# Optimization experiments

Hardware: AMD Instinct MI355X
Metric: run time of the kernel (lower is better)

Reference implementation:

```python
import jax, jax.numpy as jnp
import numpy as np

EPS = 1e-6


def softmax_kernel_transformation(data, is_query, projection_matrix):
    # data: [B,L,H,D], projection_matrix: [M,D]
    d = data.shape[-1]
    m = projection_matrix.shape[0]
    data_normalizer = 1.0 / jnp.sqrt(jnp.sqrt(jnp.float32(d)))
    data = data_normalizer * data
    ratio = 1.0 / jnp.sqrt(jnp.float32(m))
    data_dash = jnp.einsum('blhd,md->blhm', data, projection_matrix)
    diag_data = jnp.sum(jnp.square(data), axis=-1, keepdims=True) / 2.0  # [B,L,H,1]
    if is_query:
        stab = jnp.max(data_dash, axis=-1, keepdims=True)  # per-position max over M
    else:
        stab = jnp.max(data_dash, axis=(1, 3), keepdims=True)  # max over L and M
    return ratio * (jnp.exp(data_dash - diag_data - stab) + EPS)


def causal_linear_attention(qp, kp, v):
    # qp,kp: [L,B,H,M]; v: [L,B,H,D]. Sequential prefix-sum recurrence (FAVOR+ causal).
    B, H, M = qp.shape[1], qp.shape[2], qp.shape[3]
    D = v.shape[-1]
    kv0 = jnp.zeros((B, H, M, D), dtype=v.dtype)
    ks0 = jnp.zeros((B, H, M), dtype=kp.dtype)

    def step(carry, inp):
        kv_sum, k_sum = carry
        q_t, k_t, v_t = inp  # [B,H,M], [B,H,M], [B,H,D]
        kv_sum = kv_sum + jnp.einsum('bhm,bhd->bhmd', k_t, v_t)
        k_sum = k_sum + k_t
        num_t = jnp.einsum('bhmd,bhm->bhd', kv_sum, q_t)  # numerator row
        den_t = jnp.einsum('bhm,bhm->bh', q_t, k_sum)     # normalizer row
        return (kv_sum, k_sum), (num_t, den_t)

    (_, _), (num, den) = jax.lax.scan(step, (kv0, ks0), (qp, kp, v))
    return num, den  # [L,B,H,D], [L,B,H]


def favor_attention(query, key, value, projection_matrix):
    query_prime = softmax_kernel_transformation(query, True, projection_matrix)   # [B,L,H,M]
    key_prime = softmax_kernel_transformation(key, False, projection_matrix)      # [B,L,H,M]
    qp = jnp.transpose(query_prime, (1, 0, 2, 3))  # [L,B,H,M]
    kp = jnp.transpose(key_prime, (1, 0, 2, 3))
    v = jnp.transpose(value, (1, 0, 2, 3))         # [L,B,H,D]
    num, den = causal_linear_attention(qp, kp, v)
    av = jnp.transpose(num, (1, 0, 2, 3))          # [B,L,H,D]
    norm = jnp.transpose(den, (1, 0, 2))[..., None]  # [B,L,H,1]
    return av / norm


def setup_inputs() -> dict:
    B, L, H, D, M = 2, 2048, 8, 64, 128
    root = jax.random.key(0)
    kq, kk, kv, kp = jax.random.split(root, 4)
    return {
        'query': jax.random.normal(kq, (B, L, H, D), dtype=jnp.float32),
        'key': jax.random.normal(kk, (B, L, H, D), dtype=jnp.float32),
        'value': jax.random.normal(kv, (B, L, H, D), dtype=jnp.float32),
        'projection_matrix': jax.random.normal(kp, (M, D), dtype=jnp.float32),
    }


def reference(query, key, value, projection_matrix):
    return favor_attention(query, key, value, projection_matrix)
```

## Files before the change

kernel.cpp:

```cpp
#include <hip/hip_runtime.h>
#include <math.h>

typedef __attribute__((ext_vector_type(8))) short short8;
typedef __attribute__((ext_vector_type(4))) float f32x4;
typedef __attribute__((ext_vector_type(4))) unsigned short u16x4;

constexpr int B_ = 2, L_ = 2048, H_ = 8, D_ = 64, M_ = 128;
constexpr int T_ = 64;
constexpr int C_ = L_ / T_;
constexpr float DN_ = 0.35355339059327373f;
constexpr float RATIO_ = 0.08838834764831845f;
constexpr float EPSV_ = 1e-6f;
constexpr float REPS_ = RATIO_ * EPSV_;
constexpr float KEPS_ = 64.0f * REPS_;


__device__ inline unsigned short f2bf(float x) {
  const unsigned u = __float_as_uint(x);
  return (unsigned short)((u + 0x7fffu + ((u >> 16) & 1u)) >> 16);
}
__device__ inline float bf2f(unsigned short h) {
  return __uint_as_float(((unsigned)h) << 16);
}

__global__ __launch_bounds__(256) void feat_kernel(
    const float* __restrict__ q, const float* __restrict__ k,
    const float* __restrict__ P, const float* __restrict__ v,
    unsigned short* __restrict__ qp16, unsigned short* __restrict__ kp16,
    unsigned short* __restrict__ kvc16, float* __restrict__ ksc,
    unsigned short* __restrict__ vt16, float* __restrict__ blockmax,
    float* __restrict__ vsum) {
  __shared__ __align__(16) unsigned short xh_s[T_][72];
  __shared__ __align__(16) unsigned short xl_s[T_][72];
  __shared__ __align__(16) unsigned short ph_s[M_][72];
  __shared__ __align__(16) unsigned short pl_s[M_][72];
  __shared__ float diag_s[T_];
  __shared__ float wred_s[2][T_];
  __shared__ float red4_s[4];
  unsigned short (*kpT_s)[72] = ph_s;
  unsigned short (*vt_s)[72] = xh_s;

  const int bid = blockIdx.x;
  const bool isQ = bid < 512;
  const int sub = isQ ? bid : bid - 512;
  const int c = sub % C_, bh = sub / C_;
  const int b = bh >> 3, h = bh & 7;
  const float* x = isQ ? q : k;
  const int tid = threadIdx.x;
  const int w = tid >> 6, lane = tid & 63;
  const int l15 = lane & 15, l16 = lane >> 4;

  if (tid < T_) diag_s[tid] = 0.f;
  __syncthreads();
  for (int i4 = tid; i4 < T_ * 16; i4 += 256) {
    const int r = i4 >> 4, d0 = (i4 & 15) * 4;
    f32x4 t4 = *reinterpret_cast<const f32x4*>(
        &x[((size_t)(b * L_ + c * T_ + r) * H_ + h) * D_ + d0]);
    u16x4 hi, lo;
    float sq = 0.f;
#pragma unroll
    for (int j = 0; j < 4; ++j) {
      const float xv = t4[j] * DN_;
      sq += xv * xv;
      const unsigned short hb = f2bf(xv);
      hi[j] = hb;
      lo[j] = f2bf(xv - bf2f(hb));
    }
    *reinterpret_cast<u16x4*>(&xh_s[r][d0]) = hi;
    *reinterpret_cast<u16x4*>(&xl_s[r][d0]) = lo;
    atomicAdd(&diag_s[r], sq);
  }
  for (int i4 = tid; i4 < M_ * 16; i4 += 256) {
    const int m = i4 >> 4, d0 = (i4 & 15) * 4;
    const f32x4 t4 = *reinterpret_cast<const f32x4*>(&P[m * D_ + d0]);
    u16x4 hi, lo;
#pragma unroll
    for (int j = 0; j < 4; ++j) {
      const unsigned short hb = f2bf(t4[j]);
      hi[j] = hb;
      lo[j] = f2bf(t4[j] - bf2f(hb));
    }
    *reinterpret_cast<u16x4*>(&ph_s[m][d0]) = hi;
    *reinterpret_cast<u16x4*>(&pl_s[m][d0]) = lo;
  }
  __syncthreads();

  const int rblk = (w >> 1) * 32, cblk = (w & 1) * 64;
  f32x4 acc[2][4];
#pragma unroll
  for (int i = 0; i < 2; ++i)
#pragma unroll
    for (int j = 0; j < 4; ++j) acc[i][j] = {0.f, 0.f, 0.f, 0.f};
#pragma unroll
  for (int kk = 0; kk < 2; ++kk) {
    short8 ah[2], al[2], bh8[4], bl8[4];
#pragma unroll
    for (int ti = 0; ti < 2; ++ti) {
      ah[ti] = *reinterpret_cast<const short8*>(
          &xh_s[rblk + ti * 16 + l15][kk * 32 + l16 * 8]);
      al[ti] = *reinterpret_cast<const short8*>(
          &xl_s[rblk + ti * 16 + l15][kk * 32 + l16 * 8]);
    }
#pragma unroll
    for (int tj = 0; tj < 4; ++tj) {
      bh8[tj] = *reinterpret_cast<const short8*>(
          &ph_s[cblk + tj * 16 + l15][kk * 32 + l16 * 8]);
      bl8[tj] = *reinterpret_cast<const short8*>(
          &pl_s[cblk + tj * 16 + l15][kk * 32 + l16 * 8]);
    }
#pragma unroll
    for (int ti = 0; ti < 2; ++ti)
#pragma unroll
      for (int tj = 0; tj < 4; ++tj) {
        acc[ti][tj] = __builtin_amdgcn_mfma_f32_16x16x32_bf16(
            al[ti], bh8[tj], acc[ti][tj], 0, 0, 0);
        acc[ti][tj] = __builtin_amdgcn_mfma_f32_16x16x32_bf16(
            ah[ti], bl8[tj], acc[ti][tj], 0, 0, 0);
        acc[ti][tj] = __builtin_amdgcn_mfma_f32_16x16x32_bf16(
            ah[ti], bh8[tj], acc[ti][tj], 0, 0, 0);
      }
  }

  if (isQ) {
    float rmax[2][4];
#pragma unroll
    for (int ti = 0; ti < 2; ++ti)
#pragma unroll
      for (int j = 0; j < 4; ++j) {
        float m0 = fmaxf(fmaxf(acc[ti][0][j], acc[ti][1][j]),
                         fmaxf(acc[ti][2][j], acc[ti][3][j]));
#pragma unroll
        for (int off = 1; off < 16; off <<= 1)
          m0 = fmaxf(m0, __shfl_xor(m0, off, 64));
        rmax[ti][j] = m0;
      }
    if (l15 == 0) {
#pragma unroll
      for (int ti = 0; ti < 2; ++ti)
#pragma unroll
        for (int j = 0; j < 4; ++j)
          wred_s[w & 1][rblk + ti * 16 + l16 * 4 + j] = rmax[ti][j];
    }
    __syncthreads();
    unsigned short* outr = qp16 + ((size_t)bh * L_ + c * T_) * M_;
#pragma unroll
    for (int ti = 0; ti < 2; ++ti)
#pragma unroll
      for (int j = 0; j < 4; ++j) {
        const int row = rblk + ti * 16 + l16 * 4 + j;
        const float sub2 =
            0.5f * diag_s[row] + fmaxf(wred_s[0][row], wred_s[1][row]);
#pragma unroll
        for (int tj = 0; tj < 4; ++tj) {
          const int col = cblk + tj * 16 + l15;
          outr[row * M_ + col] =
              f2bf(RATIO_ * (expf(acc[ti][tj][j] - sub2) + EPSV_));
        }
      }
  } else {
    float bm = -INFINITY;
#pragma unroll
    for (int ti = 0; ti < 2; ++ti)
#pragma unroll
      for (int tj = 0; tj < 4; ++tj)
#pragma unroll
        for (int j = 0; j < 4; ++j) bm = fmaxf(bm, acc[ti][tj][j]);
#pragma unroll
    for (int off = 1; off < 64; off <<= 1)
      bm = fmaxf(bm, __shfl_xor(bm, off, 64));
    if (lane == 0) red4_s[w] = bm;
    __syncthreads();
    const float lmax =
        fmaxf(fmaxf(red4_s[0], red4_s[1]), fmaxf(red4_s[2], red4_s[3]));
    if (tid == 0) blockmax[sub] = lmax;

    unsigned short* kpr = kp16 + ((size_t)bh * L_ + c * T_) * M_;
#pragma unroll
    for (int ti = 0; ti < 2; ++ti)
#pragma unroll
      for (int j = 0; j < 4; ++j) {
        const int row = rblk + ti * 16 + l16 * 4 + j;
        const float sub2 = 0.5f * diag_s[row] + lmax;
#pragma unroll
        for (int tj = 0; tj < 4; ++tj) {
          const int col = cblk + tj * 16 + l15;
          const unsigned short us = f2bf(RATIO_ * expf(acc[ti][tj][j] - sub2));
          kpr[row * M_ + col] = us;
          kpT_s[col][row] = us;
        }
      }
    for (int i = tid; i < T_ * D_; i += 256) {
      const int t = i & 63, d = i >> 6;
      vt_s[d][t] = f2bf(v[((size_t)(b * L_ + c * T_ + t) * H_ + h) * D_ + d]);
    }
    __syncthreads();

    unsigned short* vg = vt16 + (size_t)(bh * C_ + c) * (D_ * T_);
    for (int i8 = tid; i8 < D_ * 8; i8 += 256) {
      const int d = i8 >> 3, t0 = (i8 & 7) * 8;
      *reinterpret_cast<short8*>(&vg[d * T_ + t0]) =
          *reinterpret_cast<const short8*>(&vt_s[d][t0]);
    }
    if (tid < M_) {
      float s = 0.f;
      for (int t = 0; t < T_; ++t) s += bf2f(kpT_s[tid][t]);
      ksc[(size_t)(bh * C_ + c) * M_ + tid] = s;
    }
    if (tid >= 128 && tid < 128 + D_) {
      const int d = tid - 128;
      float s = 0.f;
      for (int t = 0; t < T_; ++t) s += bf2f(vt_s[d][t]);
      vsum[(size_t)(bh * C_ + c) * D_ + d] = s;
    }
    f32x4 acc2[2][4];
#pragma unroll
    for (int i = 0; i < 2; ++i)
#pragma unroll
      for (int j = 0; j < 4; ++j) acc2[i][j] = {0.f, 0.f, 0.f, 0.f};
#pragma unroll
    for (int kk = 0; kk < 2; ++kk) {
      short8 av[2], bv[4];
#pragma unroll
      for (int ti = 0; ti < 2; ++ti)
        av[ti] = *reinterpret_cast<const short8*>(
            &vt_s[rblk + ti * 16 + l15][kk * 32 + l16 * 8]);
#pragma unroll
      for (int tj = 0; tj < 4; ++tj)
        bv[tj] = *reinterpret_cast<const short8*>(
            &kpT_s[cblk + tj * 16 + l15][kk * 32 + l16 * 8]);
#pragma unroll
      for (int ti = 0; ti < 2; ++ti)
#pragma unroll
        for (int tj = 0; tj < 4; ++tj)
          acc2[ti][tj] = __builtin_amdgcn_mfma_f32_16x16x32_bf16(
              av[ti], bv[tj], acc2[ti][tj], 0, 0, 0);
    }
    unsigned short* ob = kvc16 + (size_t)(bh * C_ + c) * (M_ * D_);
#pragma unroll
    for (int ti = 0; ti < 2; ++ti)
#pragma unroll
      for (int j = 0; j < 4; ++j) {
        const int row = rblk + ti * 16 + l16 * 4 + j;
#pragma unroll
        for (int tj = 0; tj < 4; ++tj) {
          const int col = cblk + tj * 16 + l15;
          ob[row * M_ + col] = f2bf(acc2[ti][tj][j]);
        }
      }
  }
}

__global__ __launch_bounds__(256) void prefix_kernel(
    const unsigned short* __restrict__ kvc16,
    unsigned short* __restrict__ kvp16, float* __restrict__ ksc,
    const float* __restrict__ blockmax, const float* __restrict__ vsum) {
  __shared__ float bm_s[C_];
  __shared__ float sc_s[C_];
  __shared__ float vs_s[2][C_];
  const int bid = blockIdx.x;
  const int ej = bid & 31, bh = bid >> 5;
  if (threadIdx.x < C_) bm_s[threadIdx.x] = blockmax[bh * C_ + threadIdx.x];
  if (threadIdx.x >= 64 && threadIdx.x < 64 + 2 * C_) {
    const int t = threadIdx.x - 64;
    const int ld = t >> 5, cc = t & 31;
    vs_s[ld][cc] = vsum[(size_t)(bh * C_ + cc) * D_ + ej * 2 + ld];
  }
  __syncthreads();
  if (threadIdx.x < C_) {
    float km = -INFINITY;
#pragma unroll
    for (int cc = 0; cc < C_; ++cc) km = fmaxf(km, bm_s[cc]);
    sc_s[threadIdx.x] = expf(bm_s[threadIdx.x] - km);
  }
  __syncthreads();
  const int e = ej * 256 + threadIdx.x;
  const int dl = threadIdx.x >> 7;
  float vals[C_];
#pragma unroll
  for (int cc = 0; cc < C_; ++cc)
    vals[cc] = bf2f(kvc16[(size_t)(bh * C_ + cc) * (M_ * D_) + e]) * sc_s[cc] +
               REPS_ * vs_s[dl][cc];
  float run = 0.f;
#pragma unroll
  for (int cc = 0; cc < C_; ++cc) {
    const float t = vals[cc];
    vals[cc] = run;
    run += t;
  }
#pragma unroll
  for (int cc = 0; cc < C_; ++cc)
    kvp16[(size_t)(bh * C_ + cc) * (M_ * D_) + e] = f2bf(vals[cc]);
  if (ej == 0 && threadIdx.x < M_) {
    const int m = threadIdx.x;
    float ks[C_];
#pragma unroll
    for (int cc = 0; cc < C_; ++cc)
      ks[cc] = ksc[(size_t)(bh * C_ + cc) * M_ + m] * sc_s[cc] + KEPS_;
    float rs = 0.f;
#pragma unroll
    for (int cc = 0; cc < C_; ++cc) {
      const float t = ks[cc];
      ks[cc] = rs;
      rs += t;
    }
#pragma unroll
    for (int cc = 0; cc < C_; ++cc)
      ksc[(size_t)(bh * C_ + cc) * M_ + m] = ks[cc];
  }
}

__global__ __launch_bounds__(256) void intra_kernel(
    const unsigned short* __restrict__ qp16,
    const unsigned short* __restrict__ kp16,
    const unsigned short* __restrict__ vt16,
    const unsigned short* __restrict__ kvp16, const float* __restrict__ ksp,
    const float* __restrict__ blockmax, float* __restrict__ out) {
  __shared__ __align__(16) unsigned short qp_s[T_][136];
  __shared__ __align__(16) unsigned short kp_s[T_][136];
  __shared__ __align__(16) unsigned short kvp_s[D_][136];
  __shared__ __align__(16) unsigned short S_s[T_][72];
  __shared__ __align__(16) unsigned short vt_s[D_][72];
  __shared__ float ksp_s[M_];
  __shared__ float denp_s[4][T_];
  __shared__ float qsump_s[4][T_];
  __shared__ float den_s[T_];
  __shared__ float bm_s[C_];

  const int bid = blockIdx.x;
  const int c = bid % C_, bh = bid / C_;
  const int b = bh >> 3, h = bh & 7;
  const int tid = threadIdx.x;
  const int w = tid >> 6, lane = tid & 63;
  const int l15 = lane & 15, l16 = lane >> 4;

  const unsigned short* qpt = qp16 + ((size_t)bh * L_ + c * T_) * M_;
  const unsigned short* kpt = kp16 + ((size_t)bh * L_ + c * T_) * M_;
  const unsigned short* kvt = kvp16 + (size_t)(bh * C_ + c) * (M_ * D_);
  const unsigned short* vg = vt16 + (size_t)(bh * C_ + c) * (D_ * T_);

  if (tid < C_) bm_s[tid] = blockmax[bh * C_ + tid];
  for (int i8 = tid; i8 < T_ * 16; i8 += 256) {
    const int r = i8 >> 4, m0 = (i8 & 15) * 8;
    *reinterpret_cast<short8*>(&qp_s[r][m0]) =
        *reinterpret_cast<const short8*>(&qpt[r * M_ + m0]);
    *reinterpret_cast<short8*>(&kp_s[r][m0]) =
        *reinterpret_cast<const short8*>(&kpt[r * M_ + m0]);
    *reinterpret_cast<short8*>(&kvp_s[r][m0]) =
        *reinterpret_cast<const short8*>(&kvt[r * M_ + m0]);
  }
  for (int i8 = tid; i8 < D_ * 8; i8 += 256) {
    const int d = i8 >> 3, t0 = (i8 & 7) * 8;
    *reinterpret_cast<short8*>(&vt_s[d][t0]) =
        *reinterpret_cast<const short8*>(&vg[d * T_ + t0]);
  }
  if (tid < M_) ksp_s[tid] = ksp[(size_t)(bh * C_ + c) * M_ + tid];
  __syncthreads();

  {
    const int t = lane;
    float p = 0.f;
    for (int m = w * 32; m < w * 32 + 32; ++m) p += bf2f(qp_s[t][m]);
    qsump_s[w][t] = p;
  }
  __syncthreads();

  float km = -INFINITY;
#pragma unroll
  for (int cc = 0; cc < C_; ++cc) km = fmaxf(km, bm_s[cc]);
  const float sc = expf(bm_s[c] - km);

  const int rblk = (w >> 1) * 32, cblk = (w & 1) * 32;
  f32x4 Sacc[2][2];
#pragma unroll
  for (int i = 0; i < 2; ++i)
#pragma unroll
    for (int j = 0; j < 2; ++j) Sacc[i][j] = {0.f, 0.f, 0.f, 0.f};

#pragma unroll
  for (int kk = 0; kk < 4; ++kk) {
    short8 af[2], bf[2];
#pragma unroll
    for (int ti = 0; ti < 2; ++ti)
      af[ti] = *reinterpret_cast<const short8*>(
          &qp_s[rblk + ti * 16 + l15][kk * 32 + l16 * 8]);
#pragma unroll
    for (int tj = 0; tj < 2; ++tj)
      bf[tj] = *reinterpret_cast<const short8*>(
          &kp_s[cblk + tj * 16 + l15][kk * 32 + l16 * 8]);
#pragma unroll
    for (int ti = 0; ti < 2; ++ti)
#pragma unroll
      for (int tj = 0; tj < 2; ++tj)
        Sacc[ti][tj] = __builtin_amdgcn_mfma_f32_16x16x32_bf16(
            af[ti], bf[tj], Sacc[ti][tj], 0, 0, 0);
  }
#pragma unroll
  for (int ti = 0; ti < 2; ++ti)
#pragma unroll
    for (int tj = 0; tj < 2; ++tj)
#pragma unroll
      for (int j = 0; j < 4; ++j) {
        const int row = rblk + ti * 16 + l16 * 4 + j;
        const int col = cblk + tj * 16 + l15;
        const float add = REPS_ * (qsump_s[0][row] + qsump_s[1][row] +
                                   qsump_s[2][row] + qsump_s[3][row]);
        const float sv = (col <= row) ? Sacc[ti][tj][j] * sc + add : 0.f;
        S_s[row][col] = f2bf(sv);
      }
  __syncthreads();

  {
    const int t = lane;
    float p = 0.f;
    if (w == 0) {
      for (int tp = 0; tp < 32; ++tp) p += bf2f(S_s[t][tp]);
    } else if (w == 1) {
      for (int tp = 32; tp < 64; ++tp) p += bf2f(S_s[t][tp]);
    } else if (w == 2) {
      for (int m = 0; m < 64; ++m) p += bf2f(qp_s[t][m]) * ksp_s[m];
    } else {
      for (int m = 64; m < 128; ++m) p += bf2f(qp_s[t][m]) * ksp_s[m];
    }
    denp_s[w][t] = p;
  }
  __syncthreads();
  if (tid < T_)
    den_s[tid] =
        denp_s[0][tid] + denp_s[1][tid] + denp_s[2][tid] + denp_s[3][tid];
  __syncthreads();

  const int dblk = (w & 1) * 32;
  f32x4 Nacc[2][2];
#pragma unroll
  for (int i = 0; i < 2; ++i)
#pragma unroll
    for (int j = 0; j < 2; ++j) Nacc[i][j] = {0.f, 0.f, 0.f, 0.f};

#pragma unroll
  for (int kk = 0; kk < 2; ++kk) {
    short8 af[2], bf[2];
#pragma unroll
    for (int ti = 0; ti < 2; ++ti)
      af[ti] = *reinterpret_cast<const short8*>(
          &S_s[rblk + ti * 16 + l15][kk * 32 + l16 * 8]);
#pragma unroll
    for (int tj = 0; tj < 2; ++tj)
      bf[tj] = *reinterpret_cast<const short8*>(
          &vt_s[dblk + tj * 16 + l15][kk * 32 + l16 * 8]);
#pragma unroll
    for (int ti = 0; ti < 2; ++ti)
#pragma unroll
      for (int tj = 0; tj < 2; ++tj)
        Nacc[ti][tj] = __builtin_amdgcn_mfma_f32_16x16x32_bf16(
            af[ti], bf[tj], Nacc[ti][tj], 0, 0, 0);
  }
#pragma unroll
  for (int kk = 0; kk < 4; ++kk) {
    short8 af[2], bf[2];
#pragma unroll
    for (int ti = 0; ti < 2; ++ti)
      af[ti] = *reinterpret_cast<const short8*>(
          &qp_s[rblk + ti * 16 + l15][kk * 32 + l16 * 8]);
#pragma unroll
    for (int tj = 0; tj < 2; ++tj)
      bf[tj] = *reinterpret_cast<const short8*>(
          &kvp_s[dblk + tj * 16 + l15][kk * 32 + l16 * 8]);
#pragma unroll
    for (int ti = 0; ti < 2; ++ti)
#pragma unroll
      for (int tj = 0; tj < 2; ++tj)
        Nacc[ti][tj] = __builtin_amdgcn_mfma_f32_16x16x32_bf16(
            af[ti], bf[tj], Nacc[ti][tj], 0, 0, 0);
  }

#pragma unroll
  for (int ti = 0; ti < 2; ++ti)
#pragma unroll
    for (int j = 0; j < 4; ++j) {
      const int row = rblk + ti * 16 + l16 * 4 + j;
      const float r = 1.f / den_s[row];
      float* orow = out + ((size_t)(b * L_ + c * T_ + row) * H_ + h) * D_;
#pragma unroll
      for (int tj = 0; tj < 2; ++tj) {
        const int col = dblk + tj * 16 + l15;
        orow[col] = Nacc[ti][tj][j] * r;
      }
    }
}

extern "C" void kernel_launch(void* const* d_in, const int* in_sizes, int n_in,
                              void* d_out, int out_size, void* d_ws,
                              size_t ws_size, hipStream_t stream) {
  const float* q = (const float*)d_in[0];
  const float* k = (const float*)d_in[1];
  const float* v = (const float*)d_in[2];
  const float* P = (const float*)d_in[3];
  float* out = (float*)d_out;

  float* ws = (float*)d_ws;
  float* blockmax = ws;
  float* ksp = blockmax + 512;
  float* vsum = ksp + (size_t)B_ * H_ * C_ * M_;
  unsigned short* qp16 = (unsigned short*)(vsum + (size_t)B_ * H_ * C_ * D_);
  unsigned short* kp16 = qp16 + (size_t)B_ * H_ * L_ * M_;
  unsigned short* kvc16 = kp16 + (size_t)B_ * H_ * L_ * M_;
  unsigned short* kvp16 = kvc16 + (size_t)B_ * H_ * C_ * D_ * M_;
  unsigned short* vt16 = kvp16 + (size_t)B_ * H_ * C_ * D_ * M_;

  feat_kernel<<<2 * B_ * H_ * C_, 256, 0, stream>>>(
      q, k, P, v, qp16, kp16, kvc16, ksp, vt16, blockmax, vsum);
  prefix_kernel<<<B_ * H_ * 32, 256, 0, stream>>>(kvc16, kvp16, ksp, blockmax,
                                                  vsum);
  intra_kernel<<<B_ * H_ * C_, 256, 0, stream>>>(qp16, kp16, vt16, kvp16, ksp,
                                                 blockmax, out);
}
```

Measured before the change: 48.22 us.

## Merge Q and K feature blocks, pre-split projection, stage outputs through LDS

Adds a small kernel that splits the projection matrix into bf16 hi/lo once, so the per-block split work goes away. feat_kernel now handles both the query and key tiles of a chunk in one block, with half the grid and a shared LDS buffer. It also replaces atomic diag accumulation with shuffle reductions and writes qp/kvc through LDS as vectorized stores. intra_kernel drops the LDS staging of kvp and v, reads them straight from global, and sets a launch bound for 3 blocks per SM. The merge halves parallelism and lengthens each feat block, and the global reads in the MFMA loop may be slower than LDS reads.

Measured after the change: 48.64 us. No clear change (+0.9%).

```diff
diff --git a/kernel.cpp b/kernel.cpp
--- a/kernel.cpp
+++ b/kernel.cpp
@@ -14,7 +14,6 @@
 constexpr float REPS_ = RATIO_ * EPSV_;
 constexpr float KEPS_ = 64.0f * REPS_;
 
-
 __device__ inline unsigned short f2bf(float x) {
   const unsigned u = __float_as_uint(x);
   return (unsigned short)((u + 0x7fffu + ((u >> 16) & 1u)) >> 16);
@@ -23,105 +22,106 @@
   return __uint_as_float(((unsigned)h) << 16);
 }
 
+__global__ __launch_bounds__(256) void psplit_kernel(
+    const float* __restrict__ P, unsigned short* __restrict__ Ph,
+    unsigned short* __restrict__ Pl) {
+  const int i = blockIdx.x * 256 + threadIdx.x;
+  const f32x4 t4 = *reinterpret_cast<const f32x4*>(&P[(size_t)i * 4]);
+  u16x4 hi, lo;
+#pragma unroll
+  for (int j = 0; j < 4; ++j) {
+    hi[j] = f2bf(t4[j]);
+    lo[j] = f2bf(t4[j] - bf2f(hi[j]));
+  }
+  *reinterpret_cast<u16x4*>(&Ph[(size_t)i * 4]) = hi;
+  *reinterpret_cast<u16x4*>(&Pl[(size_t)i * 4]) = lo;
+}
+
 __global__ __launch_bounds__(256) void feat_kernel(
     const float* __restrict__ q, const float* __restrict__ k,
-    const float* __restrict__ P, const float* __restrict__ v,
-    unsigned short* __restrict__ qp16, unsigned short* __restrict__ kp16,
-    unsigned short* __restrict__ kvc16, float* __restrict__ ksc,
-    unsigned short* __restrict__ vt16, float* __restrict__ blockmax,
-    float* __restrict__ vsum) {
-  __shared__ __align__(16) unsigned short xh_s[T_][72];
-  __shared__ __align__(16) unsigned short xl_s[T_][72];
-  __shared__ __align__(16) unsigned short ph_s[M_][72];
-  __shared__ __align__(16) unsigned short pl_s[M_][72];
+    const unsigned short* __restrict__ Ph, const unsigned short* __restrict__ Pl,
+    const float* __restrict__ v, unsigned short* __restrict__ qp16,
+    unsigned short* __restrict__ kp16, unsigned short* __restrict__ kvc16,
+    float* __restrict__ ksc, unsigned short* __restrict__ vt16,
+    float* __restrict__ blockmax, float* __restrict__ vsum) {
+  __shared__ __align__(16) unsigned short sm[27648];
   __shared__ float diag_s[T_];
   __shared__ float wred_s[2][T_];
   __shared__ float red4_s[4];
-  unsigned short (*kpT_s)[72] = ph_s;
-  unsigned short (*vt_s)[72] = xh_s;
-
-  const int bid = blockIdx.x;
-  const bool isQ = bid < 512;
-  const int sub = isQ ? bid : bid - 512;
+
+  const int sub = blockIdx.x;
   const int c = sub % C_, bh = sub / C_;
   const int b = bh >> 3, h = bh & 7;
-  const float* x = isQ ? q : k;
   const int tid = threadIdx.x;
   const int w = tid >> 6, lane = tid & 63;
   const int l15 = lane & 15, l16 = lane >> 4;
-
-  if (tid < T_) diag_s[tid] = 0.f;
-  __syncthreads();
-  for (int i4 = tid; i4 < T_ * 16; i4 += 256) {
-    const int r = i4 >> 4, d0 = (i4 & 15) * 4;
-    f32x4 t4 = *reinterpret_cast<const f32x4*>(
-        &x[((size_t)(b * L_ + c * T_ + r) * H_ + h) * D_ + d0]);
-    u16x4 hi, lo;
-    float sq = 0.f;
-#pragma unroll
-    for (int j = 0; j < 4; ++j) {
-      const float xv = t4[j] * DN_;
-      sq += xv * xv;
-      const unsigned short hb = f2bf(xv);
-      hi[j] = hb;
-      lo[j] = f2bf(xv - bf2f(hb));
-    }
-    *reinterpret_cast<u16x4*>(&xh_s[r][d0]) = hi;
-    *reinterpret_cast<u16x4*>(&xl_s[r][d0]) = lo;
-    atomicAdd(&diag_s[r], sq);
-  }
-  for (int i4 = tid; i4 < M_ * 16; i4 += 256) {
-    const int m = i4 >> 4, d0 = (i4 & 15) * 4;
-    const f32x4 t4 = *reinterpret_cast<const f32x4*>(&P[m * D_ + d0]);
-    u16x4 hi, lo;
-#pragma unroll
-    for (int j = 0; j < 4; ++j) {
-      const unsigned short hb = f2bf(t4[j]);
-      hi[j] = hb;
-      lo[j] = f2bf(t4[j] - bf2f(hb));
-    }
-    *reinterpret_cast<u16x4*>(&ph_s[m][d0]) = hi;
-    *reinterpret_cast<u16x4*>(&pl_s[m][d0]) = lo;
-  }
-  __syncthreads();
-
   const int rblk = (w >> 1) * 32, cblk = (w & 1) * 64;
+
+  for (int i8 = tid; i8 < M_ * 8; i8 += 256) {
+    const int m = i8 >> 3, d0 = (i8 & 7) * 8;
+    *reinterpret_cast<short8*>(&sm[9216 + m * 72 + d0]) =
+        *reinterpret_cast<const short8*>(&Ph[m * D_ + d0]);
+    *reinterpret_cast<short8*>(&sm[18432 + m * 72 + d0]) =
+        *reinterpret_cast<const short8*>(&Pl[m * D_ + d0]);
+  }
+
+#define STAGE_X(xptr)                                                         \
+  for (int i4 = tid; i4 < T_ * 16; i4 += 256) {                               \
+    const int r = i4 >> 4, d0 = (i4 & 15) * 4;                                \
+    f32x4 t4 = *reinterpret_cast<const f32x4*>(                               \
+        &(xptr)[((size_t)(b * L_ + c * T_ + r) * H_ + h) * D_ + d0]);         \
+    u16x4 hi, lo;                                                             \
+    float sq = 0.f;                                                           \
+    _Pragma("unroll") for (int j = 0; j < 4; ++j) {                           \
+      const float xv = t4[j] * DN_;                                           \
+      sq += xv * xv;                                                          \
+      const unsigned short hb = f2bf(xv);                                     \
+      hi[j] = hb;                                                             \
+      lo[j] = f2bf(xv - bf2f(hb));                                            \
+    }                                                                         \
+    *reinterpret_cast<u16x4*>(&sm[r * 72 + d0]) = hi;                         \
+    *reinterpret_cast<u16x4*>(&sm[4608 + r * 72 + d0]) = lo;                  \
+    _Pragma("unroll") for (int off = 1; off < 16; off <<= 1)                  \
+        sq += __shfl_xor(sq, off, 64);                                        \
+    if ((tid & 15) == 0) diag_s[r] = sq;                                      \
+  }
+
+#define DASH_MFMA(accv)                                                       \
+  _Pragma("unroll") for (int kk = 0; kk < 2; ++kk) {                          \
+    short8 ah[2], al[2], bh8[4], bl8[4];                                      \
+    _Pragma("unroll") for (int ti = 0; ti < 2; ++ti) {                        \
+      ah[ti] = *reinterpret_cast<const short8*>(                              \
+          &sm[(rblk + ti * 16 + l15) * 72 + kk * 32 + l16 * 8]);              \
+      al[ti] = *reinterpret_cast<const short8*>(                              \
+          &sm[4608 + (rblk + ti * 16 + l15) * 72 + kk * 32 + l16 * 8]);       \
+    }                                                                         \
+    _Pragma("unroll") for (int tj = 0; tj < 4; ++tj) {                        \
+      bh8[tj] = *reinterpret_cast<const short8*>(                             \
+          &sm[9216 + (cblk + tj * 16 + l15) * 72 + kk * 32 + l16 * 8]);       \
+      bl8[tj] = *reinterpret_cast<const short8*>(                             \
+          &sm[18432 + (cblk + tj * 16 + l15) * 72 + kk * 32 + l16 * 8]);      \
+    }                                                                         \
+    _Pragma("unroll") for (int ti = 0; ti < 2; ++ti)                          \
+        _Pragma("unroll") for (int tj = 0; tj < 4; ++tj) {                    \
+      accv[ti][tj] = __builtin_amdgcn_mfma_f32_16x16x32_bf16(                 \
+          al[ti], bh8[tj], accv[ti][tj], 0, 0, 0);                            \
+      accv[ti][tj] = __builtin_amdgcn_mfma_f32_16x16x32_bf16(                 \
+          ah[ti], bl8[tj], accv[ti][tj], 0, 0, 0);                            \
+      accv[ti][tj] = __builtin_amdgcn_mfma_f32_16x16x32_bf16(                 \
+          ah[ti], bh8[tj], accv[ti][tj], 0, 0, 0);                            \
+    }                                                                         \
+  }
+
+  STAGE_X(q);
+  __syncthreads();
   f32x4 acc[2][4];
 #pragma unroll
   for (int i = 0; i < 2; ++i)
 #pragma unroll
     for (int j = 0; j < 4; ++j) acc[i][j] = {0.f, 0.f, 0.f, 0.f};
-#pragma unroll
-  for (int kk = 0; kk < 2; ++kk) {
-    short8 ah[2], al[2], bh8[4], bl8[4];
-#pragma unroll
-    for (int ti = 0; ti < 2; ++ti) {
-      ah[ti] = *reinterpret_cast<const short8*>(
-          &xh_s[rblk + ti * 16 + l15][kk * 32 + l16 * 8]);
-      al[ti] = *reinterpret_cast<const short8*>(
-          &xl_s[rblk + ti * 16 + l15][kk * 32 + l16 * 8]);
-    }
-#pragma unroll
-    for (int tj = 0; tj < 4; ++tj) {
-      bh8[tj] = *reinterpret_cast<const short8*>(
-          &ph_s[cblk + tj * 16 + l15][kk * 32 + l16 * 8]);
-      bl8[tj] = *reinterpret_cast<const short8*>(
-          &pl_s[cblk + tj * 16 + l15][kk * 32 + l16 * 8]);
-    }
-#pragma unroll
-    for (int ti = 0; ti < 2; ++ti)
-#pragma unroll
-      for (int tj = 0; tj < 4; ++tj) {
-        acc[ti][tj] = __builtin_amdgcn_mfma_f32_16x16x32_bf16(
-            al[ti], bh8[tj], acc[ti][tj], 0, 0, 0);
-        acc[ti][tj] = __builtin_amdgcn_mfma_f32_16x16x32_bf16(
-            ah[ti], bl8[tj], acc[ti][tj], 0, 0, 0);
-        acc[ti][tj] = __builtin_amdgcn_mfma_f32_16x16x32_bf16(
-            ah[ti], bh8[tj], acc[ti][tj], 0, 0, 0);
-      }
-  }
-
-  if (isQ) {
+  DASH_MFMA(acc);
+
+  {
     float rmax[2][4];
 #pragma unroll
     for (int ti = 0; ti < 2; ++ti)
@@ -142,7 +142,6 @@
           wred_s[w & 1][rblk + ti * 16 + l16 * 4 + j] = rmax[ti][j];
     }
     __syncthreads();
-    unsigned short* outr = qp16 + ((size_t)bh * L_ + c * T_) * M_;
 #pragma unroll
     for (int ti = 0; ti < 2; ++ti)
 #pragma unroll
@@ -153,101 +152,136 @@
 #pragma unroll
         for (int tj = 0; tj < 4; ++tj) {
           const int col = cblk + tj * 16 + l15;
-          outr[row * M_ + col] =
+          sm[row * 136 + col] =
               f2bf(RATIO_ * (expf(acc[ti][tj][j] - sub2) + EPSV_));
         }
       }
-  } else {
-    float bm = -INFINITY;
+    __syncthreads();
+    unsigned short* outr = qp16 + ((size_t)bh * L_ + c * T_) * M_;
+    for (int i8 = tid; i8 < T_ * 16; i8 += 256) {
+      const int row = i8 >> 4, m0 = (i8 & 15) * 8;
+      *reinterpret_cast<short8*>(&outr[row * M_ + m0]) =
+          *reinterpret_cast<const short8*>(&sm[row * 136 + m0]);
+    }
+  }
+  __syncthreads();
+
+  STAGE_X(k);
+  __syncthreads();
+#pragma unroll
+  for (int i = 0; i < 2; ++i)
+#pragma unroll
+    for (int j = 0; j < 4; ++j) acc[i][j] = {0.f, 0.f, 0.f, 0.f};
+  DASH_MFMA(acc);
+
+  float bm = -INFINITY;
+#pragma unroll
+  for (int ti = 0; ti < 2; ++ti)
+#pragma unroll
+    for (int tj = 0; tj < 4; ++tj)
+#pragma unroll
+      for (int j = 0; j < 4; ++j) bm = fmaxf(bm, acc[ti][tj][j]);
+#pragma unroll
+  for (int off = 1; off < 64; off <<= 1) bm = fmaxf(bm, __shfl_xor(bm, off, 64));
+  if (lane == 0) red4_s[w] = bm;
+  __syncthreads();
+  const float lmax =
+      fmaxf(fmaxf(red4_s[0], red4_s[1]), fmaxf(red4_s[2], red4_s[3]));
+  if (tid == 0) blockmax[sub] = lmax;
+
+  unsigned short* kpr = kp16 + ((size_t)bh * L_ + c * T_) * M_;
+#pragma unroll
+  for (int ti = 0; ti < 2; ++ti)
+#pragma unroll
+    for (int j = 0; j < 4; ++j) {
+      const int row = rblk + ti * 16 + l16 * 4 + j;
+      const float sub2 = 0.5f * diag_s[row] + lmax;
+#pragma unroll
+      for (int tj = 0; tj < 4; ++tj) {
+        const int col = cblk + tj * 16 + l15;
+        const unsigned short us = f2bf(RATIO_ * expf(acc[ti][tj][j] - sub2));
+        kpr[row * M_ + col] = us;
+        sm[9216 + col * 72 + row] = us;
+      }
+    }
+  for (int i = tid; i < T_ * D_; i += 256) {
+    const int t = i & 63, d = i >> 6;
+    sm[d * 72 + t] =
+        f2bf(v[((size_t)(b * L_ + c * T_ + t) * H_ + h) * D_ + d]);
+  }
+  __syncthreads();
+
+  unsigned short* vg = vt16 + (size_t)(bh * C_ + c) * (D_ * T_);
+  for (int i8 = tid; i8 < D_ * 8; i8 += 256) {
+    const int d = i8 >> 3, t0 = (i8 & 7) * 8;
+    *reinterpret_cast<short8*>(&vg[d * T_ + t0]) =
+        *reinterpret_cast<const short8*>(&sm[d * 72 + t0]);
+  }
+  if (tid < M_) {
+    float s = 0.f;
+#pragma unroll
+    for (int t8 = 0; t8 < 8; ++t8) {
+      const short8 h8 =
+          *reinterpret_cast<const short8*>(&sm[9216 + tid * 72 + t8 * 8]);
+#pragma unroll
+      for (int j = 0; j < 8; ++j) s += bf2f((unsigned short)h8[j]);
+    }
+    ksc[(size_t)(bh * C_ + c) * M_ + tid] = s;
+  }
+  if (tid >= 128 && tid < 128 + D_) {
+    const int d = tid - 128;
+    float s = 0.f;
+#pragma unroll
+    for (int t8 = 0; t8 < 8; ++t8) {
+      const short8 h8 = *reinterpret_cast<const short8*>(&sm[d * 72 + t8 * 8]);
+#pragma unroll
+      for (int j = 0; j < 8; ++j) s += bf2f((unsigned short)h8[j]);
+    }
+    vsum[(size_t)(bh * C_ + c) * D_ + d] = s;
+  }
+  f32x4 acc2[2][4];
+#pragma unroll
+  for (int i = 0; i < 2; ++i)
+#pragma unroll
+    for (int j = 0; j < 4; ++j) acc2[i][j] = {0.f, 0.f, 0.f, 0.f};
+#pragma unroll
+  for (int kk = 0; kk < 2; ++kk) {
+    short8 av[2], bv[4];
+#pragma unroll
+    for (int ti = 0; ti < 2; ++ti)
+      av[ti] = *reinterpret_cast<const short8*>(
+          &sm[(rblk + ti * 16 + l15) * 72 + kk * 32 + l16 * 8]);
+#pragma unroll
+    for (int tj = 0; tj < 4; ++tj)
+      bv[tj] = *reinterpret_cast<const short8*>(
+          &sm[9216 + (cblk + tj * 16 + l15) * 72 + kk * 32 + l16 * 8]);
 #pragma unroll
     for (int ti = 0; ti < 2; ++ti)
 #pragma unroll
       for (int tj = 0; tj < 4; ++tj)
-#pragma unroll
-        for (int j = 0; j < 4; ++j) bm = fmaxf(bm, acc[ti][tj][j]);
-#pragma unroll
-    for (int off = 1; off < 64; off <<= 1)
-      bm = fmaxf(bm, __shfl_xor(bm, off, 64));
-    if (lane == 0) red4_s[w] = bm;
-    __syncthreads();
-    const float lmax =
-        fmaxf(fmaxf(red4_s[0], red4_s[1]), fmaxf(red4_s[2], red4_s[3]));
-    if (tid == 0) blockmax[sub] = lmax;
-
-    unsigned short* kpr = kp16 + ((size_t)bh * L_ + c * T_) * M_;
-#pragma unroll
-    for (int ti = 0; ti < 2; ++ti)
-#pragma unroll
-      for (int j = 0; j < 4; ++j) {
-        const int row = rblk + ti * 16 + l16 * 4 + j;
-        const float sub2 = 0.5f * diag_s[row] + lmax;
-#pragma unroll
-        for (int tj = 0; tj < 4; ++tj) {
-          const int col = cblk + tj * 16 + l15;
-          const unsigned short us = f2bf(RATIO_ * expf(acc[ti][tj][j] - sub2));
-          kpr[row * M_ + col] = us;
-          kpT_s[col][row] = us;
-        }
+        acc2[ti][tj] = __builtin_amdgcn_mfma_f32_16x16x32_bf16(
+            av[ti], bv[tj], acc2[ti][tj], 0, 0, 0);
+  }
+#pragma unroll
+  for (int ti = 0; ti < 2; ++ti)
+#pragma unroll
+    for (int j = 0; j < 4; ++j) {
+      const int row = rblk + ti * 16 + l16 * 4 + j;
+#pragma unroll
+      for (int tj = 0; tj < 4; ++tj) {
+        const int col = cblk + tj * 16 + l15;
+        sm[18432 + row * 136 + col] = f2bf(acc2[ti][tj][j]);
       }
-    for (int i = tid; i < T_ * D_; i += 256) {
-      const int t = i & 63, d = i >> 6;
-      vt_s[d][t] = f2bf(v[((size_t)(b * L_ + c * T_ + t) * H_ + h) * D_ + d]);
-    }
-    __syncthreads();
-
-    unsigned short* vg = vt16 + (size_t)(bh * C_ + c) * (D_ * T_);
-    for (int i8 = tid; i8 < D_ * 8; i8 += 256) {
-      const int d = i8 >> 3, t0 = (i8 & 7) * 8;
-      *reinterpret_cast<short8*>(&vg[d * T_ + t0]) =
-          *reinterpret_cast<const short8*>(&vt_s[d][t0]);
-    }
-    if (tid < M_) {
-      float s = 0.f;
-      for (int t = 0; t < T_; ++t) s += bf2f(kpT_s[tid][t]);
-      ksc[(size_t)(bh * C_ + c) * M_ + tid] = s;
-    }
-    if (tid >= 128 && tid < 128 + D_) {
-      const int d = tid - 128;
-      float s = 0.f;
-      for (int t = 0; t < T_; ++t) s += bf2f(vt_s[d][t]);
-      vsum[(size_t)(bh * C_ + c) * D_ + d] = s;
-    }
-    f32x4 acc2[2][4];
-#pragma unroll
-    for (int i = 0; i < 2; ++i)
-#pragma unroll
-      for (int j = 0; j < 4; ++j) acc2[i][j] = {0.f, 0.f, 0.f, 0.f};
-#pragma unroll
-    for (int kk = 0; kk < 2; ++kk) {
-      short8 av[2], bv[4];
-#pragma unroll
-      for (int ti = 0; ti < 2; ++ti)
-        av[ti] = *reinterpret_cast<const short8*>(
-            &vt_s[rblk + ti * 16 + l15][kk * 32 + l16 * 8]);
-#pragma unroll
-      for (int tj = 0; tj < 4; ++tj)
-        bv[tj] = *reinterpret_cast<const short8*>(
-            &kpT_s[cblk + tj * 16 + l15][kk * 32 + l16 * 8]);
-#pragma unroll
-      for (int ti = 0; ti < 2; ++ti)
-#pragma unroll
-        for (int tj = 0; tj < 4; ++tj)
-          acc2[ti][tj] = __builtin_amdgcn_mfma_f32_16x16x32_bf16(
-              av[ti], bv[tj], acc2[ti][tj], 0, 0, 0);
-    }
-    unsigned short* ob = kvc16 + (size_t)(bh * C_ + c) * (M_ * D_);
-#pragma unroll
-    for (int ti = 0; ti < 2; ++ti)
-#pragma unroll
-      for (int j = 0; j < 4; ++j) {
-        const int row = rblk + ti * 16 + l16 * 4 + j;
-#pragma unroll
-        for (int tj = 0; tj < 4; ++tj) {
-          const int col = cblk + tj * 16 + l15;
-          ob[row * M_ + col] = f2bf(acc2[ti][tj][j]);
-        }
-      }
-  }
+    }
+  __syncthreads();
+  unsigned short* ob = kvc16 + (size_t)(bh * C_ + c) * (M_ * D_);
+  for (int i8 = tid; i8 < D_ * 16; i8 += 256) {
+    const int d = i8 >> 4, m0 = (i8 & 15) * 8;
+    *reinterpret_cast<short8*>(&ob[d * M_ + m0]) =
+        *reinterpret_cast<const short8*>(&sm[18432 + d * 136 + m0]);
+  }
+#undef STAGE_X
+#undef DASH_MFMA
 }
 
 __global__ __launch_bounds__(256) void prefix_kernel(
@@ -309,7 +343,7 @@
   }
 }
 
-__global__ __launch_bounds__(256) void intra_kernel(
+__global__ __launch_bounds__(256, 3) void intra_kernel(
     const unsigned short* __restrict__ qp16,
     const unsigned short* __restrict__ kp16,
     const unsigned short* __restrict__ vt16,
@@ -317,13 +351,11 @@
     const float* __restrict__ blockmax, float* __restrict__ out) {
   __shared__ __align__(16) unsigned short qp_s[T_][136];
   __shared__ __align__(16) unsigned short kp_s[T_][136];
-  __shared__ __align__(16) unsigned short kvp_s[D_][136];
   __shared__ __align__(16) unsigned short S_s[T_][72];
-  __shared__ __align__(16) unsigned short vt_s[D_][72];
   __shared__ float ksp_s[M_];
   __shared__ float denp_s[4][T_];
-  __shared__ float qsump_s[4][T_];
   __shared__ float den_s[T_];
+  __shared__ float qsum_s[T_];
   __shared__ float bm_s[C_];
 
   const int bid = blockIdx.x;
@@ -345,22 +377,23 @@
         *reinterpret_cast<const short8*>(&qpt[r * M_ + m0]);
     *reinterpret_cast<short8*>(&kp_s[r][m0]) =
         *reinterpret_cast<const short8*>(&kpt[r * M_ + m0]);
-    *reinterpret_cast<short8*>(&kvp_s[r][m0]) =
-        *reinterpret_cast<const short8*>(&kvt[r * M_ + m0]);
-  }
-  for (int i8 = tid; i8 < D_ * 8; i8 += 256) {
-    const int d = i8 >> 3, t0 = (i8 & 7) * 8;
-    *reinterpret_cast<short8*>(&vt_s[d][t0]) =
-        *reinterpret_cast<const short8*>(&vg[d * T_ + t0]);
   }
   if (tid < M_) ksp_s[tid] = ksp[(size_t)(bh * C_ + c) * M_ + tid];
   __syncthreads();
 
   {
-    const int t = lane;
+    const int row = w * 16 + (lane >> 2), mseg = (lane & 3) * 32;
     float p = 0.f;
-    for (int m = w * 32; m < w * 32 + 32; ++m) p += bf2f(qp_s[t][m]);
-    qsump_s[w][t] = p;
+#pragma unroll
+    for (int u = 0; u < 4; ++u) {
+      const short8 h8 =
+          *reinterpret_cast<const short8*>(&qp_s[row][mseg + u * 8]);
+#pragma unroll
+      for (int j = 0; j < 8; ++j) p += bf2f((unsigned short)h8[j]);
+    }
+    p += __shfl_xor(p, 1, 64);
+    p += __shfl_xor(p, 2, 64);
+    if ((lane & 3) == 0) qsum_s[row] = p;
   }
   __syncthreads();
 
@@ -402,8 +435,7 @@
       for (int j = 0; j < 4; ++j) {
         const int row = rblk + ti * 16 + l16 * 4 + j;
         const int col = cblk + tj * 16 + l15;
-        const float add = REPS_ * (qsump_s[0][row] + qsump_s[1][row] +
-                                   qsump_s[2][row] + qsump_s[3][row]);
+        const float add = REPS_ * qsum_s[row];
         const float sv = (col <= row) ? Sacc[ti][tj][j] * sc + add : 0.f;
         S_s[row][col] = f2bf(sv);
       }
@@ -446,7 +478,7 @@
 #pragma unroll
     for (int tj = 0; tj < 2; ++tj)
       bf[tj] = *reinterpret_cast<const short8*>(
-          &vt_s[dblk + tj * 16 + l15][kk * 32 + l16 * 8]);
+          &vg[(dblk + tj * 16 + l15) * T_ + kk * 32 + l16 * 8]);
 #pragma unroll
     for (int ti = 0; ti < 2; ++ti)
 #pragma unroll
@@ -464,7 +496,7 @@
 #pragma unroll
     for (int tj = 0; tj < 2; ++tj)
       bf[tj] = *reinterpret_cast<const short8*>(
-          &kvp_s[dblk + tj * 16 + l15][kk * 32 + l16 * 8]);
+          &kvt[(dblk + tj * 16 + l15) * M_ + kk * 32 + l16 * 8]);
 #pragma unroll
     for (int ti = 0; ti < 2; ++ti)
 #pragma unroll
@@ -501,14 +533,18 @@
   float* blockmax = ws;
   float* ksp = blockmax + 512;
   float* vsum = ksp + (size_t)B_ * H_ * C_ * M_;
-  unsigned short* qp16 = (unsigned short*)(vsum + (size_t)B_ * H_ * C_ * D_);
+  unsigned short* Ph16 = (unsigned short*)(vsum + (size_t)B_ * H_ * C_ * D_);
+  unsigned short* Pl16 = Ph16 + M_ * D_;
+  unsigned short* qp16 = Pl16 + M_ * D_;
   unsigned short* kp16 = qp16 + (size_t)B_ * H_ * L_ * M_;
   unsigned short* kvc16 = kp16 + (size_t)B_ * H_ * L_ * M_;
   unsigned short* kvp16 = kvc16 + (size_t)B_ * H_ * C_ * D_ * M_;
   unsigned short* vt16 = kvp16 + (size_t)B_ * H_ * C_ * D_ * M_;
 
-  feat_kernel<<<2 * B_ * H_ * C_, 256, 0, stream>>>(
-      q, k, P, v, qp16, kp16, kvc16, ksp, vt16, blockmax, vsum);
+  psplit_kernel<<<M_ * D_ / 1024, 256, 0, stream>>>(P, Ph16, Pl16);
+  feat_kernel<<<B_ * H_ * C_, 256, 0, stream>>>(q, k, Ph16, Pl16, v, qp16,
+                                                kp16, kvc16, ksp, vt16,
+                                                blockmax, vsum);
   prefix_kernel<<<B_ * H_ * 32, 256, 0, stream>>>(kvc16, kvp16, ksp, blockmax,
                                                   vsum);
   intra_kernel<<<B_ * H_ * C_, 256, 0, stream>>>(qp16, kp16, vt16, kvp16, ksp,
```
